# Kernel optimization log

Measured on AMD Instinct MI355X. Metric: run time of the kernel, lower is better.

The kernel has to match this reference:

```python
import jax, jax.numpy as jnp
import numpy as np

N_BASIS = 16


def _kan_layer(x, coeffs, centers):
    # x: [b, in], coeffs: [out, in, n], centers: [n]
    mu = jnp.mean(x, axis=0)
    sd = jnp.std(x, axis=0, ddof=1)  # torch.std is unbiased by default
    xn = jnp.clip((x - mu) / (sd + 1e-6), -3.0, 3.0)
    # Gaussian RBF expansion: [b, in, n]
    basis = jnp.exp(-((xn[..., None] - centers) ** 2) / 0.5)
    return jnp.einsum('bin,oin->bo', basis, coeffs)


def setup_inputs() -> dict:
    key = jax.random.key(0)
    ks = jax.random.split(key, 6)
    B, IN, H = 16384, 256, 512
    return {
        'x': jax.random.normal(ks[0], (B, IN), jnp.float32),
        'coeffs1': jax.random.normal(ks[1], (H, IN, N_BASIS), jnp.float32) * 0.1,
        'coeffs2': jax.random.normal(ks[2], (H, H, N_BASIS), jnp.float32) * 0.1,
        'coeffs3': jax.random.normal(ks[3], (1, H, N_BASIS), jnp.float32) * 0.1,
        'skip_w': jax.random.normal(ks[4], (1, IN), jnp.float32) * 0.05,
        'skip_b': jnp.zeros((1,), jnp.float32),
    }


def reference(x, coeffs1, coeffs2, coeffs3, skip_w, skip_b):
    centers = jnp.linspace(-2.0, 2.0, N_BASIS).astype(x.dtype)
    h = jnp.tanh(_kan_layer(x, coeffs1, centers))
    h = jnp.tanh(_kan_layer(h, coeffs2, centers))
    out = _kan_layer(h, coeffs3, centers)[:, 0]  # squeeze(-1)
    skip = (x @ skip_w.T + skip_b)[:, 0]
    return out + skip
```

## Files before the change

kernel.cpp:

```cpp
#include <hip/hip_runtime.h>
#include <cstdint>
#include <cstddef>

typedef __attribute__((ext_vector_type(8))) _Float16 half8;
typedef __attribute__((ext_vector_type(4))) _Float16 half4;
typedef __attribute__((ext_vector_type(2))) __fp16   fp16x2;
typedef __attribute__((ext_vector_type(4))) float    floatx4;

static constexpr int B_ROWS = 16384;
static constexpr int IN_DIM = 256;
static constexpr int H_DIM  = 512;
static constexpr int NB     = 16;

__device__ __forceinline__ float fast_tanh(float x) {
  float ax = fabsf(x);
  float e  = __expf(2.0f * ax);
  float t  = 1.0f - 2.0f / (e + 1.0f);
  return copysignf(t, x);
}

__device__ __forceinline__ void gld16(const void* g, void* l) {
  __builtin_amdgcn_global_load_lds(
      (const __attribute__((address_space(1))) unsigned int*)g,
      (__attribute__((address_space(3))) unsigned int*)l, 16, 0, 0);
}

__global__ __launch_bounds__(256) void prep_k(const float* __restrict__ c1, _Float16* __restrict__ d1, size_t n41,
                                              const float* __restrict__ c2, _Float16* __restrict__ d2, size_t n42,
                                              const float* __restrict__ X,
                                              float* __restrict__ ps, float* __restrict__ ps2) {
  const int bx = blockIdx.x;
  if (bx < 128) {
    int c     = (bx & 3) * 64 + (threadIdx.x & 63);
    int chunk = threadIdx.x >> 6;
    int seg   = bx >> 2;
    int r0    = seg * 512;
    double s = 0.0, s2 = 0.0;
    for (int r = r0 + chunk; r < r0 + 512; r += 4) {
      float v = X[(size_t)r * IN_DIM + c];
      s += v; s2 += (double)v * (double)v;
    }
    __shared__ float Ls[256], Ls2[256];
    Ls[threadIdx.x] = (float)s; Ls2[threadIdx.x] = (float)s2;
    __syncthreads();
    if (chunk == 0) {
      int cl = threadIdx.x;
      float a  = Ls[cl]  + Ls[cl + 64]  + Ls[cl + 128]  + Ls[cl + 192];
      float b  = Ls2[cl] + Ls2[cl + 64] + Ls2[cl + 128] + Ls2[cl + 192];
      ps [(size_t)seg * IN_DIM + c] = a;
      ps2[(size_t)seg * IN_DIM + c] = b;
    }
  } else {
    size_t tot = n41 + n42;
    int nb_blocks = gridDim.x - 128;
    for (size_t i = (size_t)(bx - 128) * 256 + threadIdx.x; i < tot;
         i += (size_t)nb_blocks * 256) {
      const float4* sp; half4* dp; size_t j;
      if (i < n41) { sp = (const float4*)c1; dp = (half4*)d1; j = i; }
      else         { sp = (const float4*)c2; dp = (half4*)d2; j = i - n41; }
      float4 v = sp[j];
      int nb = (int)((j << 2) & 15);
      half4 r;
      float e0 = -2.f + (float)(nb + 0) * (4.f / 15.f);
      float e1 = -2.f + (float)(nb + 1) * (4.f / 15.f);
      float e2 = -2.f + (float)(nb + 2) * (4.f / 15.f);
      float e3 = -2.f + (float)(nb + 3) * (4.f / 15.f);
      r[0] = (_Float16)(v.x * __expf(-2.f * e0 * e0));
      r[1] = (_Float16)(v.y * __expf(-2.f * e1 * e1));
      r[2] = (_Float16)(v.z * __expf(-2.f * e2 * e2));
      r[3] = (_Float16)(v.w * __expf(-2.f * e3 * e3));
      dp[j] = r;
    }
  }
}

__global__ void stats_final_k(const float* __restrict__ ps,
                              const float* __restrict__ ps2,
                              int segs, int cols, int rows,
                              float* __restrict__ nmi, float* __restrict__ isd) {
  int c = blockIdx.x * blockDim.x + threadIdx.x;
  if (c >= cols) return;
  double s = 0.0, s2 = 0.0;
  for (int g = 0; g < segs; g++) { s += ps[(size_t)g * cols + c]; s2 += ps2[(size_t)g * cols + c]; }
  double mean = s / rows;
  double var  = (s2 - s * s / rows) / (rows - 1);
  if (var < 0.0) var = 0.0;
  float sd = (float)sqrt(var);
  float iv = 1.0f / (sd + 1e-6f);
  isd[c] = iv;
  nmi[c] = -(float)mean * iv;
}

__global__ __launch_bounds__(512, 4) void kan_gemm_fused(const float* __restrict__ X,
                                                         const float* __restrict__ nmi,
                                                         const float* __restrict__ isd,
                                                         const _Float16* __restrict__ Bm,
                                                         float* __restrict__ Hout,
                                                         float* __restrict__ psum,
                                                         float* __restrict__ psum2,
                                                         int C) {
  const int K = C << 4;
  const int steps = K >> 6;
  __shared__ __align__(16) _Float16 As[2][128 * 64];
  __shared__ __align__(16) _Float16 Bs[3][128 * 64];
  const int tid  = threadIdx.x;
  const int w = tid >> 6, lane = tid & 63;
  const int wm = w & 1, wn = w >> 1;
  const int lrow = lane & 15, quad = lane >> 4;
  const int row0 = blockIdx.x * 128;
  const int col0 = blockIdx.y * 128;

  const int s_row = tid >> 3;
  const int s_sl  = tid & 7;
  const int s_seg = s_sl ^ ((s_row >> 1) & 7);
  const _Float16* gB = Bm + (size_t)(col0 + s_row) * K + s_seg * 8;

  const int erow = tid & 127;
  const int eh   = tid >> 7;
  const float* xp  = X   + (size_t)(row0 + erow) * C + eh;
  const float* mup = nmi + eh;
  const float* isp = isd + eh;

  floatx4 acc[4][2] = {};

  auto expand_store = [&](float xr, float ii, float bb, int bufi) {
    float xn = fminf(fmaxf(fmaf(xr, ii, bb), -3.f), 3.f);
    float Wv = __expf(fmaf(-2.f, xn, -8.f) * xn);
    float g  = __expf((16.f / 15.f) * xn);
    float g2 = g * g, g4 = g2 * g2, g8 = g4 * g4;
    fp16x2 gg = __builtin_amdgcn_cvt_pkrtz(g2, g2);
    union { fp16x2 q[4]; half8 v8; } u0, u1;
    u0.q[0] = __builtin_amdgcn_cvt_pkrtz(Wv, Wv * g);
    u0.q[1] = u0.q[0] * gg;
    u0.q[2] = u0.q[1] * gg;
    u0.q[3] = u0.q[2] * gg;
    float W8 = Wv * g8;
    u1.q[0] = __builtin_amdgcn_cvt_pkrtz(W8, W8 * g);
    u1.q[1] = u1.q[0] * gg;
    u1.q[2] = u1.q[1] * gg;
    u1.q[3] = u1.q[2] * gg;
    int ks0 = 2 * eh;
    *(half8*)&As[bufi][(size_t)(ks0 * 128 + erow) * 8]       = u0.v8;
    *(half8*)&As[bufi][(size_t)((ks0 + 1) * 128 + erow) * 8] = u1.v8;
  };

  float x0 = xp[0];
  float a0 = isp[0];
  float b0 = mup[0];
  gld16(gB, &Bs[0][(size_t)tid * 8]);
  gld16(gB + (size_t)64 * K, &Bs[0][(size_t)(tid + 512) * 8]);
  __builtin_amdgcn_sched_barrier(0);
  gld16(gB + 64, &Bs[1][(size_t)tid * 8]);
  gld16(gB + 64 + (size_t)64 * K, &Bs[1][(size_t)(tid + 512) * 8]);
  __builtin_amdgcn_sched_barrier(0);
  float xv = xp[4];
  float av = isp[4];
  float bv = mup[4];
  expand_store(x0, a0, b0, 0);
  asm volatile("s_waitcnt vmcnt(0)" ::: "memory");
  asm volatile("s_waitcnt lgkmcnt(0)" ::: "memory");
  __builtin_amdgcn_s_barrier();
  __builtin_amdgcn_sched_barrier(0);

  int bcur = 0;
  for (int k = 0; k < steps; k++) {
    const int abuf = k & 1;
    const bool more  = (k + 1 < steps);
    const bool more2 = (k + 2 < steps);
    const int b2 = (bcur == 0) ? 2 : bcur - 1;
    if (more2) {
      gld16(gB + (size_t)(k + 2) * 64, &Bs[b2][(size_t)tid * 8]);
      gld16(gB + (size_t)(k + 2) * 64 + (size_t)64 * K, &Bs[b2][(size_t)(tid + 512) * 8]);
      __builtin_amdgcn_sched_barrier(0);
    }
    half8 af0[4], bf0[2];
#pragma unroll
    for (int t = 0; t < 4; t++) {
      int arow = wm * 64 + t * 16 + lrow;
      af0[t] = *(const half8*)&As[abuf][(size_t)(quad * 128 + arow) * 8];
    }
#pragma unroll
    for (int t = 0; t < 2; t++) {
      int brow = wn * 32 + t * 16 + lrow;
      int bchunk = brow * 8 + (quad ^ ((brow >> 1) & 7));
      bf0[t] = *(const half8*)&Bs[bcur][(size_t)bchunk * 8];
    }
    __builtin_amdgcn_s_setprio(1);
#pragma unroll
    for (int tm = 0; tm < 4; tm++)
#pragma unroll
      for (int tn = 0; tn < 2; tn++)
        acc[tm][tn] = __builtin_amdgcn_mfma_f32_16x16x32_f16(af0[tm], bf0[tn], acc[tm][tn], 0, 0, 0);
    __builtin_amdgcn_s_setprio(0);
    if (more) {
      expand_store(xv, av, bv, abuf ^ 1);
      if (more2) {
        xv = xp[4 * (k + 2)];
        av = isp[4 * (k + 2)];
        bv = mup[4 * (k + 2)];
      }
    }
    half8 af1[4], bf1[2];
#pragma unroll
    for (int t = 0; t < 4; t++) {
      int arow = wm * 64 + t * 16 + lrow;
      af1[t] = *(const half8*)&As[abuf][(size_t)((4 + quad) * 128 + arow) * 8];
    }
#pragma unroll
    for (int t = 0; t < 2; t++) {
      int brow = wn * 32 + t * 16 + lrow;
      int bchunk = brow * 8 + ((4 + quad) ^ ((brow >> 1) & 7));
      bf1[t] = *(const half8*)&Bs[bcur][(size_t)bchunk * 8];
    }
    __builtin_amdgcn_s_setprio(1);
#pragma unroll
    for (int tm = 0; tm < 4; tm++)
#pragma unroll
      for (int tn = 0; tn < 2; tn++)
        acc[tm][tn] = __builtin_amdgcn_mfma_f32_16x16x32_f16(af1[tm], bf1[tn], acc[tm][tn], 0, 0, 0);
    __builtin_amdgcn_s_setprio(0);
    asm volatile("s_waitcnt lgkmcnt(0)" ::: "memory");
    __builtin_amdgcn_s_barrier();
    __builtin_amdgcn_sched_barrier(0);
    bcur = (bcur == 2) ? 0 : bcur + 1;
  }

  float* Rs1 = reinterpret_cast<float*>(&As[0][0]);
  float* Rs2 = Rs1 + 256;
  float s1[2] = {0.f, 0.f}, s2v[2] = {0.f, 0.f};
#pragma unroll
  for (int tm = 0; tm < 4; tm++) {
#pragma unroll
    for (int tn = 0; tn < 2; tn++) {
      int gcol = col0 + wn * 32 + tn * 16 + lrow;
#pragma unroll
      for (int r = 0; r < 4; r++) {
        int grow = row0 + wm * 64 + tm * 16 + quad * 4 + r;
        float v = fast_tanh(acc[tm][tn][r]);
        Hout[(size_t)grow * H_DIM + gcol] = v;
        s1[tn] += v; s2v[tn] += v * v;
      }
    }
  }
#pragma unroll
  for (int tn = 0; tn < 2; tn++) {
    s1[tn]  += __shfl_xor(s1[tn], 16);  s1[tn]  += __shfl_xor(s1[tn], 32);
    s2v[tn] += __shfl_xor(s2v[tn], 16); s2v[tn] += __shfl_xor(s2v[tn], 32);
  }
  if (quad == 0) {
#pragma unroll
    for (int tn = 0; tn < 2; tn++) {
      Rs1[wm * 128 + wn * 32 + tn * 16 + lrow] = s1[tn];
      Rs2[wm * 128 + wn * 32 + tn * 16 + lrow] = s2v[tn];
    }
  }
  asm volatile("s_waitcnt lgkmcnt(0)" ::: "memory");
  __builtin_amdgcn_s_barrier();
  __builtin_amdgcn_sched_barrier(0);
  if (tid < 128) {
    psum [(size_t)blockIdx.x * H_DIM + col0 + tid] = Rs1[tid] + Rs1[128 + tid];
    psum2[(size_t)blockIdx.x * H_DIM + col0 + tid] = Rs2[tid] + Rs2[128 + tid];
  }
}

__global__ __launch_bounds__(256) void layer3_k(const float* __restrict__ H2,
                                                const float* __restrict__ nmi,
                                                const float* __restrict__ isd,
                                                const float* __restrict__ C3,
                                                const float* __restrict__ X,
                                                const float* __restrict__ SW,
                                                const float* __restrict__ SB,
                                                float* __restrict__ OUT) {
  int w = threadIdx.x >> 6, lane = threadIdx.x & 63;
  float Kn[NB];
#pragma unroll
  for (int n = 0; n < NB; n++) {
    float c = -2.f + (float)n * (4.f / 15.f);
    Kn[n] = __expf(-2.f * c * c);
  }
  float sb0 = SB[0];
  int row_base = blockIdx.x * 16 + w * 4;
  for (int r = 0; r < 4; r++) {
    int row = row_base + r;
    float s = 0.f;
#pragma unroll
    for (int j = 0; j < 8; j++) {
      int i = lane + 64 * j;
      float hv = H2[(size_t)row * H_DIM + i];
      float xn = fminf(fmaxf(fmaf(hv, isd[i], nmi[i]), -3.f), 3.f);
      float Wf = __expf(fmaf(-2.f, xn, -8.f) * xn);
      float gf = __expf((16.f / 15.f) * xn);
      const floatx4* cp = (const floatx4*)(C3 + (size_t)i * NB);
      floatx4 c0 = cp[0], c1 = cp[1], c2 = cp[2], c3 = cp[3];
      float p = Wf;
#pragma unroll
      for (int n = 0; n < 4; n++) { s += p * Kn[n]      * c0[n]; p *= gf; }
#pragma unroll
      for (int n = 0; n < 4; n++) { s += p * Kn[n + 4]  * c1[n]; p *= gf; }
#pragma unroll
      for (int n = 0; n < 4; n++) { s += p * Kn[n + 8]  * c2[n]; p *= gf; }
#pragma unroll
      for (int n = 0; n < 4; n++) { s += p * Kn[n + 12] * c3[n]; p *= gf; }
    }
#pragma unroll
    for (int j = 0; j < 4; j++) {
      int i = lane + 64 * j;
      s += X[(size_t)row * IN_DIM + i] * SW[i];
    }
#pragma unroll
    for (int off = 32; off > 0; off >>= 1) s += __shfl_down(s, off);
    if (lane == 0) OUT[row] = s + sb0;
  }
}

extern "C" void kernel_launch(void* const* d_in, const int* in_sizes, int n_in,
                              void* d_out, int out_size, void* d_ws, size_t ws_size,
                              hipStream_t stream) {
  const float* x  = (const float*)d_in[0];
  const float* c1 = (const float*)d_in[1];
  const float* c2 = (const float*)d_in[2];
  const float* c3 = (const float*)d_in[3];
  const float* sw = (const float*)d_in[4];
  const float* sb = (const float*)d_in[5];
  float* out = (float*)d_out;

  const int B = B_ROWS, IN = IN_DIM, H = H_DIM;

  char* ws = (char*)d_ws;
  size_t off = 0;
  auto alloc = [&](size_t bytes) -> void* {
    void* p = ws + off;
    off += (bytes + 255) & ~(size_t)255;
    return p;
  };
  _Float16* C1h = (_Float16*)alloc((size_t)H * IN * NB * 2);
  _Float16* C2h = (_Float16*)alloc((size_t)H * H  * NB * 2);
  float* H1 = (float*)alloc((size_t)B * H * 4);
  float* H2 = (float*)alloc((size_t)B * H * 4);
  float* ps  = (float*)alloc(128 * 512 * 4);
  float* ps2 = (float*)alloc(128 * 512 * 4);
  float* nmi = (float*)alloc(512 * 4);
  float* isd = (float*)alloc(512 * 4);

  prep_k<<<128 + 1024, 256, 0, stream>>>(c1, C1h, (size_t)H * IN * NB / 4,
                                         c2, C2h, (size_t)H * H * NB / 4,
                                         x, ps, ps2);
  stats_final_k<<<1, 256, 0, stream>>>(ps, ps2, 32, IN, B, nmi, isd);

  kan_gemm_fused<<<dim3(B / 128, 4), 512, 0, stream>>>(x, nmi, isd, C1h, H1, ps, ps2, IN);
  stats_final_k<<<2, 256, 0, stream>>>(ps, ps2, 128, H, B, nmi, isd);

  kan_gemm_fused<<<dim3(B / 128, 4), 512, 0, stream>>>(H1, nmi, isd, C2h, H2, ps, ps2, H);
  stats_final_k<<<2, 256, 0, stream>>>(ps, ps2, 128, H, B, nmi, isd);

  layer3_k<<<B / 16, 256, 0, stream>>>(H2, nmi, isd, c3, x, sw, sb, out);
}
```

Baseline: 457.6 us.

## Fold column-stats finalization into GEMM prologue and load B fragments directly to registers

Removes the separate stats_final_k launches before each GEMM. Each GEMM block now reduces the partial sums itself into a shared normalization table, using separate partial-sum buffers per layer so nothing is overwritten. The B-operand path drops the LDS triple buffer and async global-to-LDS copies, and instead loads B fragments straight from global memory into registers, double-buffered across a 2-step unrolled loop. This cuts launch overhead and LDS traffic, but every block repeats the stats reduction (up to 128 segments per column) and B fragment loads are no longer shared through LDS across waves.

```diff
diff --git a/kernel.cpp b/kernel.cpp
--- a/kernel.cpp
+++ b/kernel.cpp
@@ -17,12 +17,6 @@
   float e  = __expf(2.0f * ax);
   float t  = 1.0f - 2.0f / (e + 1.0f);
   return copysignf(t, x);
-}
-
-__device__ __forceinline__ void gld16(const void* g, void* l) {
-  __builtin_amdgcn_global_load_lds(
-      (const __attribute__((address_space(1))) unsigned int*)g,
-      (__attribute__((address_space(3))) unsigned int*)l, 16, 0, 0);
 }
 
 __global__ __launch_bounds__(256) void prep_k(const float* __restrict__ c1, _Float16* __restrict__ d1, size_t n41,
@@ -92,8 +86,9 @@
 }
 
 __global__ __launch_bounds__(512, 4) void kan_gemm_fused(const float* __restrict__ X,
-                                                         const float* __restrict__ nmi,
-                                                         const float* __restrict__ isd,
+                                                         const float* __restrict__ psin,
+                                                         const float* __restrict__ ps2in,
+                                                         int segs,
                                                          const _Float16* __restrict__ Bm,
                                                          float* __restrict__ Hout,
                                                          float* __restrict__ psum,
@@ -102,7 +97,7 @@
   const int K = C << 4;
   const int steps = K >> 6;
   __shared__ __align__(16) _Float16 As[2][128 * 64];
-  __shared__ __align__(16) _Float16 Bs[3][128 * 64];
+  __shared__ float2 SN[512];
   const int tid  = threadIdx.x;
   const int w = tid >> 6, lane = tid & 63;
   const int wm = w & 1, wn = w >> 1;
@@ -110,21 +105,25 @@
   const int row0 = blockIdx.x * 128;
   const int col0 = blockIdx.y * 128;
 
-  const int s_row = tid >> 3;
-  const int s_sl  = tid & 7;
-  const int s_seg = s_sl ^ ((s_row >> 1) & 7);
-  const _Float16* gB = Bm + (size_t)(col0 + s_row) * K + s_seg * 8;
+  const _Float16* gBf = Bm + (size_t)(col0 + wn * 32 + lrow) * K + quad * 8;
 
   const int erow = tid & 127;
   const int eh   = tid >> 7;
-  const float* xp  = X   + (size_t)(row0 + erow) * C + eh;
-  const float* mup = nmi + eh;
-  const float* isp = isd + eh;
+  const float* xp = X + (size_t)(row0 + erow) * C + eh;
 
   floatx4 acc[4][2] = {};
-
-  auto expand_store = [&](float xr, float ii, float bb, int bufi) {
-    float xn = fminf(fmaxf(fmaf(xr, ii, bb), -3.f), 3.f);
+  half8 bfA[4], bfB[4];
+
+  auto loadB = [&](int k, half8 (&bf)[4]) {
+#pragma unroll
+    for (int ks = 0; ks < 2; ks++)
+#pragma unroll
+      for (int t = 0; t < 2; t++)
+        bf[ks * 2 + t] = *(const half8*)(gBf + (size_t)t * 16 * K + (size_t)k * 64 + ks * 32);
+  };
+
+  auto expand_store = [&](float xr, float2 sn, int bufi) {
+    float xn = fminf(fmaxf(fmaf(xr, sn.x, sn.y), -3.f), 3.f);
     float Wv = __expf(fmaf(-2.f, xn, -8.f) * xn);
     float g  = __expf((16.f / 15.f) * xn);
     float g2 = g * g, g4 = g2 * g2, g8 = g4 * g4;
@@ -144,85 +143,66 @@
     *(half8*)&As[bufi][(size_t)((ks0 + 1) * 128 + erow) * 8] = u1.v8;
   };
 
+  auto mfma_half = [&](const half8 (&bf)[4], int ks, int abuf_) {
+    half8 af[4];
+#pragma unroll
+    for (int t = 0; t < 4; t++) {
+      int arow = wm * 64 + t * 16 + lrow;
+      af[t] = *(const half8*)&As[abuf_][(size_t)((ks * 4 + quad) * 128 + arow) * 8];
+    }
+    __builtin_amdgcn_s_setprio(1);
+#pragma unroll
+    for (int tm = 0; tm < 4; tm++)
+#pragma unroll
+      for (int tn = 0; tn < 2; tn++)
+        acc[tm][tn] = __builtin_amdgcn_mfma_f32_16x16x32_f16(af[tm], bf[ks * 2 + tn], acc[tm][tn], 0, 0, 0);
+    __builtin_amdgcn_s_setprio(0);
+  };
+
+  loadB(0, bfA);
+  for (int c = tid; c < C; c += 512) {
+    double s = 0.0, s2 = 0.0;
+    for (int g = 0; g < segs; g++) {
+      s  += psin [(size_t)g * C + c];
+      s2 += ps2in[(size_t)g * C + c];
+    }
+    double mean = s / B_ROWS;
+    double var  = (s2 - s * s / B_ROWS) / (B_ROWS - 1);
+    if (var < 0.0) var = 0.0;
+    float iv = 1.0f / ((float)sqrt(var) + 1e-6f);
+    SN[c] = make_float2(iv, -(float)mean * iv);
+  }
   float x0 = xp[0];
-  float a0 = isp[0];
-  float b0 = mup[0];
-  gld16(gB, &Bs[0][(size_t)tid * 8]);
-  gld16(gB + (size_t)64 * K, &Bs[0][(size_t)(tid + 512) * 8]);
-  __builtin_amdgcn_sched_barrier(0);
-  gld16(gB + 64, &Bs[1][(size_t)tid * 8]);
-  gld16(gB + 64 + (size_t)64 * K, &Bs[1][(size_t)(tid + 512) * 8]);
-  __builtin_amdgcn_sched_barrier(0);
-  float xv = xp[4];
-  float av = isp[4];
-  float bv = mup[4];
-  expand_store(x0, a0, b0, 0);
-  asm volatile("s_waitcnt vmcnt(0)" ::: "memory");
   asm volatile("s_waitcnt lgkmcnt(0)" ::: "memory");
   __builtin_amdgcn_s_barrier();
   __builtin_amdgcn_sched_barrier(0);
-
-  int bcur = 0;
-  for (int k = 0; k < steps; k++) {
-    const int abuf = k & 1;
-    const bool more  = (k + 1 < steps);
-    const bool more2 = (k + 2 < steps);
-    const int b2 = (bcur == 0) ? 2 : bcur - 1;
-    if (more2) {
-      gld16(gB + (size_t)(k + 2) * 64, &Bs[b2][(size_t)tid * 8]);
-      gld16(gB + (size_t)(k + 2) * 64 + (size_t)64 * K, &Bs[b2][(size_t)(tid + 512) * 8]);
-      __builtin_amdgcn_sched_barrier(0);
-    }
-    half8 af0[4], bf0[2];
-#pragma unroll
-    for (int t = 0; t < 4; t++) {
-      int arow = wm * 64 + t * 16 + lrow;
-      af0[t] = *(const half8*)&As[abuf][(size_t)(quad * 128 + arow) * 8];
-    }
-#pragma unroll
-    for (int t = 0; t < 2; t++) {
-      int brow = wn * 32 + t * 16 + lrow;
-      int bchunk = brow * 8 + (quad ^ ((brow >> 1) & 7));
-      bf0[t] = *(const half8*)&Bs[bcur][(size_t)bchunk * 8];
-    }
-    __builtin_amdgcn_s_setprio(1);
-#pragma unroll
-    for (int tm = 0; tm < 4; tm++)
-#pragma unroll
-      for (int tn = 0; tn < 2; tn++)
-        acc[tm][tn] = __builtin_amdgcn_mfma_f32_16x16x32_f16(af0[tm], bf0[tn], acc[tm][tn], 0, 0, 0);
-    __builtin_amdgcn_s_setprio(0);
-    if (more) {
-      expand_store(xv, av, bv, abuf ^ 1);
-      if (more2) {
-        xv = xp[4 * (k + 2)];
-        av = isp[4 * (k + 2)];
-        bv = mup[4 * (k + 2)];
-      }
-    }
-    half8 af1[4], bf1[2];
-#pragma unroll
-    for (int t = 0; t < 4; t++) {
-      int arow = wm * 64 + t * 16 + lrow;
-      af1[t] = *(const half8*)&As[abuf][(size_t)((4 + quad) * 128 + arow) * 8];
-    }
-#pragma unroll
-    for (int t = 0; t < 2; t++) {
-      int brow = wn * 32 + t * 16 + lrow;
-      int bchunk = brow * 8 + ((4 + quad) ^ ((brow >> 1) & 7));
-      bf1[t] = *(const half8*)&Bs[bcur][(size_t)bchunk * 8];
-    }
-    __builtin_amdgcn_s_setprio(1);
-#pragma unroll
-    for (int tm = 0; tm < 4; tm++)
-#pragma unroll
-      for (int tn = 0; tn < 2; tn++)
-        acc[tm][tn] = __builtin_amdgcn_mfma_f32_16x16x32_f16(af1[tm], bf1[tn], acc[tm][tn], 0, 0, 0);
-    __builtin_amdgcn_s_setprio(0);
+  float2 sn0 = SN[eh];
+  float xv   = xp[4];
+  float2 snv = SN[4 + eh];
+  expand_store(x0, sn0, 0);
+  asm volatile("s_waitcnt lgkmcnt(0)" ::: "memory");
+  __builtin_amdgcn_s_barrier();
+  __builtin_amdgcn_sched_barrier(0);
+
+  for (int k = 0; k < steps; k += 2) {
+    loadB(k + 1, bfB);
+    mfma_half(bfA, 0, 0);
+    expand_store(xv, snv, 1);
+    if (k + 2 < steps) { xv = xp[4 * (k + 2)]; snv = SN[4 * (k + 2) + eh]; }
+    mfma_half(bfA, 1, 0);
     asm volatile("s_waitcnt lgkmcnt(0)" ::: "memory");
     __builtin_amdgcn_s_barrier();
     __builtin_amdgcn_sched_barrier(0);
-    bcur = (bcur == 2) ? 0 : bcur + 1;
+    if (k + 2 < steps) loadB(k + 2, bfA);
+    mfma_half(bfB, 0, 1);
+    if (k + 2 < steps) {
+      expand_store(xv, snv, 0);
+      if (k + 3 < steps) { xv = xp[4 * (k + 3)]; snv = SN[4 * (k + 3) + eh]; }
+    }
+    mfma_half(bfB, 1, 1);
+    asm volatile("s_waitcnt lgkmcnt(0)" ::: "memory");
+    __builtin_amdgcn_s_barrier();
+    __builtin_amdgcn_sched_barrier(0);
   }
 
   float* Rs1 = reinterpret_cast<float*>(&As[0][0]);
@@ -337,21 +317,23 @@
   _Float16* C2h = (_Float16*)alloc((size_t)H * H  * NB * 2);
   float* H1 = (float*)alloc((size_t)B * H * 4);
   float* H2 = (float*)alloc((size_t)B * H * 4);
-  float* ps  = (float*)alloc(128 * 512 * 4);
-  float* ps2 = (float*)alloc(128 * 512 * 4);
+  float* psX  = (float*)alloc(32 * 256 * 4);
+  float* ps2X = (float*)alloc(32 * 256 * 4);
+  float* psA  = (float*)alloc(128 * 512 * 4);
+  float* ps2A = (float*)alloc(128 * 512 * 4);
+  float* psB  = (float*)alloc(128 * 512 * 4);
+  float* ps2B = (float*)alloc(128 * 512 * 4);
   float* nmi = (float*)alloc(512 * 4);
   float* isd = (float*)alloc(512 * 4);
 
   prep_k<<<128 + 1024, 256, 0, stream>>>(c1, C1h, (size_t)H * IN * NB / 4,
                                          c2, C2h, (size_t)H * H * NB / 4,
-                                         x, ps, ps2);
-  stats_final_k<<<1, 256, 0, stream>>>(ps, ps2, 32, IN, B, nmi, isd);
-
-  kan_gemm_fused<<<dim3(B / 128, 4), 512, 0, stream>>>(x, nmi, isd, C1h, H1, ps, ps2, IN);
-  stats_final_k<<<2, 256, 0, stream>>>(ps, ps2, 128, H, B, nmi, isd);
-
-  kan_gemm_fused<<<dim3(B / 128, 4), 512, 0, stream>>>(H1, nmi, isd, C2h, H2, ps, ps2, H);
-  stats_final_k<<<2, 256, 0, stream>>>(ps, ps2, 128, H, B, nmi, isd);
-
+                                         x, psX, ps2X);
+
+  kan_gemm_fused<<<dim3(B / 128, 4), 512, 0, stream>>>(x, psX, ps2X, 32, C1h, H1, psA, ps2A, IN);
+
+  kan_gemm_fused<<<dim3(B / 128, 4), 512, 0, stream>>>(H1, psA, ps2A, 128, C2h, H2, psB, ps2B, H);
+
+  stats_final_k<<<2, 256, 0, stream>>>(psB, ps2B, 128, H, B, nmi, isd);
   layer3_k<<<B / 16, 256, 0, stream>>>(H2, nmi, isd, c3, x, sw, sb, out);
 }
```

After: 658.0 us. 1.44x slower.

## Split K across warp groups with larger per-warp tiles and LDS reduction

Applied to the files above, without the earlier changes.

Reorganizes the 8 warps of the fused KAN GEMM into two K-halves, each covering the full 128x128 block as 2x2 warps with 64x64 tiles. This replaces the previous 2x4 warp grid with 64x32 tiles, so each warp now reuses more A/B fragments per MFMA, lowering LDS reads per flop. The second K-half writes its accumulators to LDS and the first adds them before the tanh and stats epilogue. In exchange it doubles the accumulator registers (64 floats per lane), which may cut occupancy under launch_bounds(512,4), and adds a 64KB LDS reduction step plus extra barrier work in the epilogue.

```diff
diff --git a/kernel.cpp b/kernel.cpp
--- a/kernel.cpp
+++ b/kernel.cpp
@@ -101,14 +101,16 @@
                                                          int C) {
   const int K = C << 4;
   const int steps = K >> 6;
-  __shared__ __align__(16) _Float16 As[2][128 * 64];
-  __shared__ __align__(16) _Float16 Bs[3][128 * 64];
+  __shared__ __align__(16) unsigned char LDSB[81920];
+  _Float16* const Asb = reinterpret_cast<_Float16*>(LDSB);
+  _Float16* const Bsb = reinterpret_cast<_Float16*>(LDSB + 32768);
   const int tid  = threadIdx.x;
   const int w = tid >> 6, lane = tid & 63;
-  const int wm = w & 1, wn = w >> 1;
+  const int wm = w & 1, wn = (w >> 1) & 1, ksw = w >> 2;
   const int lrow = lane & 15, quad = lane >> 4;
   const int row0 = blockIdx.x * 128;
   const int col0 = blockIdx.y * 128;
+  const int kq = ksw * 4 + quad;
 
   const int s_row = tid >> 3;
   const int s_sl  = tid & 7;
@@ -121,7 +123,7 @@
   const float* mup = nmi + eh;
   const float* isp = isd + eh;
 
-  floatx4 acc[4][2] = {};
+  floatx4 acc[4][4] = {};
 
   auto expand_store = [&](float xr, float ii, float bb, int bufi) {
     float xn = fminf(fmaxf(fmaf(xr, ii, bb), -3.f), 3.f);
@@ -140,18 +142,18 @@
     u1.q[2] = u1.q[1] * gg;
     u1.q[3] = u1.q[2] * gg;
     int ks0 = 2 * eh;
-    *(half8*)&As[bufi][(size_t)(ks0 * 128 + erow) * 8]       = u0.v8;
-    *(half8*)&As[bufi][(size_t)((ks0 + 1) * 128 + erow) * 8] = u1.v8;
+    *(half8*)&Asb[(size_t)bufi * 8192 + (size_t)(ks0 * 128 + erow) * 8]       = u0.v8;
+    *(half8*)&Asb[(size_t)bufi * 8192 + (size_t)((ks0 + 1) * 128 + erow) * 8] = u1.v8;
   };
 
   float x0 = xp[0];
   float a0 = isp[0];
   float b0 = mup[0];
-  gld16(gB, &Bs[0][(size_t)tid * 8]);
-  gld16(gB + (size_t)64 * K, &Bs[0][(size_t)(tid + 512) * 8]);
-  __builtin_amdgcn_sched_barrier(0);
-  gld16(gB + 64, &Bs[1][(size_t)tid * 8]);
-  gld16(gB + 64 + (size_t)64 * K, &Bs[1][(size_t)(tid + 512) * 8]);
+  gld16(gB, &Bsb[(size_t)tid * 8]);
+  gld16(gB + (size_t)64 * K, &Bsb[(size_t)(tid + 512) * 8]);
+  __builtin_amdgcn_sched_barrier(0);
+  gld16(gB + 64, &Bsb[8192 + (size_t)tid * 8]);
+  gld16(gB + 64 + (size_t)64 * K, &Bsb[8192 + (size_t)(tid + 512) * 8]);
   __builtin_amdgcn_sched_barrier(0);
   float xv = xp[4];
   float av = isp[4];
@@ -169,28 +171,29 @@
     const bool more2 = (k + 2 < steps);
     const int b2 = (bcur == 0) ? 2 : bcur - 1;
     if (more2) {
-      gld16(gB + (size_t)(k + 2) * 64, &Bs[b2][(size_t)tid * 8]);
-      gld16(gB + (size_t)(k + 2) * 64 + (size_t)64 * K, &Bs[b2][(size_t)(tid + 512) * 8]);
+      gld16(gB + (size_t)(k + 2) * 64, &Bsb[(size_t)b2 * 8192 + (size_t)tid * 8]);
+      gld16(gB + (size_t)(k + 2) * 64 + (size_t)64 * K,
+            &Bsb[(size_t)b2 * 8192 + (size_t)(tid + 512) * 8]);
       __builtin_amdgcn_sched_barrier(0);
     }
-    half8 af0[4], bf0[2];
+    half8 af[4], bf[4];
 #pragma unroll
     for (int t = 0; t < 4; t++) {
       int arow = wm * 64 + t * 16 + lrow;
-      af0[t] = *(const half8*)&As[abuf][(size_t)(quad * 128 + arow) * 8];
-    }
-#pragma unroll
-    for (int t = 0; t < 2; t++) {
-      int brow = wn * 32 + t * 16 + lrow;
-      int bchunk = brow * 8 + (quad ^ ((brow >> 1) & 7));
-      bf0[t] = *(const half8*)&Bs[bcur][(size_t)bchunk * 8];
+      af[t] = *(const half8*)&Asb[(size_t)abuf * 8192 + (size_t)(kq * 128 + arow) * 8];
+    }
+#pragma unroll
+    for (int t = 0; t < 4; t++) {
+      int brow = wn * 64 + t * 16 + lrow;
+      int bchunk = brow * 8 + (kq ^ ((brow >> 1) & 7));
+      bf[t] = *(const half8*)&Bsb[(size_t)bcur * 8192 + (size_t)bchunk * 8];
     }
     __builtin_amdgcn_s_setprio(1);
 #pragma unroll
-    for (int tm = 0; tm < 4; tm++)
-#pragma unroll
-      for (int tn = 0; tn < 2; tn++)
-        acc[tm][tn] = __builtin_amdgcn_mfma_f32_16x16x32_f16(af0[tm], bf0[tn], acc[tm][tn], 0, 0, 0);
+    for (int tm = 0; tm < 2; tm++)
+#pragma unroll
+      for (int tn = 0; tn < 4; tn++)
+        acc[tm][tn] = __builtin_amdgcn_mfma_f32_16x16x32_f16(af[tm], bf[tn], acc[tm][tn], 0, 0, 0);
     __builtin_amdgcn_s_setprio(0);
     if (more) {
       expand_store(xv, av, bv, abuf ^ 1);
@@ -200,24 +203,12 @@
         bv = mup[4 * (k + 2)];
       }
     }
-    half8 af1[4], bf1[2];
-#pragma unroll
-    for (int t = 0; t < 4; t++) {
-      int arow = wm * 64 + t * 16 + lrow;
-      af1[t] = *(const half8*)&As[abuf][(size_t)((4 + quad) * 128 + arow) * 8];
-    }
-#pragma unroll
-    for (int t = 0; t < 2; t++) {
-      int brow = wn * 32 + t * 16 + lrow;
-      int bchunk = brow * 8 + ((4 + quad) ^ ((brow >> 1) & 7));
-      bf1[t] = *(const half8*)&Bs[bcur][(size_t)bchunk * 8];
-    }
     __builtin_amdgcn_s_setprio(1);
 #pragma unroll
-    for (int tm = 0; tm < 4; tm++)
-#pragma unroll
-      for (int tn = 0; tn < 2; tn++)
-        acc[tm][tn] = __builtin_amdgcn_mfma_f32_16x16x32_f16(af1[tm], bf1[tn], acc[tm][tn], 0, 0, 0);
+    for (int tm = 2; tm < 4; tm++)
+#pragma unroll
+      for (int tn = 0; tn < 4; tn++)
+        acc[tm][tn] = __builtin_amdgcn_mfma_f32_16x16x32_f16(af[tm], bf[tn], acc[tm][tn], 0, 0, 0);
     __builtin_amdgcn_s_setprio(0);
     asm volatile("s_waitcnt lgkmcnt(0)" ::: "memory");
     __builtin_amdgcn_s_barrier();
@@ -225,33 +216,52 @@
     bcur = (bcur == 2) ? 0 : bcur + 1;
   }
 
-  float* Rs1 = reinterpret_cast<float*>(&As[0][0]);
+  float* MB = reinterpret_cast<float*>(LDSB);
+  const int p = wm * 2 + wn;
+  asm volatile("s_waitcnt vmcnt(0)" ::: "memory");
+  if (ksw == 1) {
+    float* dst = MB + (size_t)p * 4096;
+#pragma unroll
+    for (int tm = 0; tm < 4; tm++)
+#pragma unroll
+      for (int tn = 0; tn < 4; tn++)
+        *(floatx4*)&dst[((tm * 4 + tn) * 64 + lane) * 4] = acc[tm][tn];
+  }
+  asm volatile("s_waitcnt lgkmcnt(0)" ::: "memory");
+  __builtin_amdgcn_s_barrier();
+  __builtin_amdgcn_sched_barrier(0);
+
+  float* Rs1 = MB + 16384;
   float* Rs2 = Rs1 + 256;
-  float s1[2] = {0.f, 0.f}, s2v[2] = {0.f, 0.f};
-#pragma unroll
-  for (int tm = 0; tm < 4; tm++) {
-#pragma unroll
-    for (int tn = 0; tn < 2; tn++) {
-      int gcol = col0 + wn * 32 + tn * 16 + lrow;
-#pragma unroll
-      for (int r = 0; r < 4; r++) {
-        int grow = row0 + wm * 64 + tm * 16 + quad * 4 + r;
-        float v = fast_tanh(acc[tm][tn][r]);
-        Hout[(size_t)grow * H_DIM + gcol] = v;
-        s1[tn] += v; s2v[tn] += v * v;
+  if (ksw == 0) {
+    const float* src = MB + (size_t)p * 4096;
+    float s1[4] = {0.f, 0.f, 0.f, 0.f}, s2v[4] = {0.f, 0.f, 0.f, 0.f};
+#pragma unroll
+    for (int tm = 0; tm < 4; tm++) {
+#pragma unroll
+      for (int tn = 0; tn < 4; tn++) {
+        floatx4 other = *(const floatx4*)&src[((tm * 4 + tn) * 64 + lane) * 4];
+        int gcol = col0 + wn * 64 + tn * 16 + lrow;
+#pragma unroll
+        for (int r = 0; r < 4; r++) {
+          int grow = row0 + wm * 64 + tm * 16 + quad * 4 + r;
+          float v = fast_tanh(acc[tm][tn][r] + other[r]);
+          Hout[(size_t)grow * H_DIM + gcol] = v;
+          s1[tn] += v; s2v[tn] += v * v;
+        }
       }
     }
-  }
-#pragma unroll
-  for (int tn = 0; tn < 2; tn++) {
-    s1[tn]  += __shfl_xor(s1[tn], 16);  s1[tn]  += __shfl_xor(s1[tn], 32);
-    s2v[tn] += __shfl_xor(s2v[tn], 16); s2v[tn] += __shfl_xor(s2v[tn], 32);
-  }
-  if (quad == 0) {
-#pragma unroll
-    for (int tn = 0; tn < 2; tn++) {
-      Rs1[wm * 128 + wn * 32 + tn * 16 + lrow] = s1[tn];
-      Rs2[wm * 128 + wn * 32 + tn * 16 + lrow] = s2v[tn];
+#pragma unroll
+    for (int tn = 0; tn < 4; tn++) {
+      s1[tn]  += __shfl_xor(s1[tn], 16);  s1[tn]  += __shfl_xor(s1[tn], 32);
+      s2v[tn] += __shfl_xor(s2v[tn], 16); s2v[tn] += __shfl_xor(s2v[tn], 32);
+    }
+    if (quad == 0) {
+#pragma unroll
+      for (int tn = 0; tn < 4; tn++) {
+        Rs1[wm * 128 + wn * 64 + tn * 16 + lrow] = s1[tn];
+        Rs2[wm * 128 + wn * 64 + tn * 16 + lrow] = s2v[tn];
+      }
     }
   }
   asm volatile("s_waitcnt lgkmcnt(0)" ::: "memory");
```

Result: no change. 457.3 us (-0.1%).
